# Optimization experiments

Measured on AMD Instinct MI355X. Metric: run time of the kernel, lower is better.

The kernel has to match this reference:

```python
import jax, jax.numpy as jnp
import numpy as np
from jax import lax

B, DZ, H, U, T, V = 256, 512, 512, 16, 16, 512  # batch, latent, lstm hidden, segments, steps/segment, vocab


def setup_inputs() -> dict:
    key = jax.random.key(0)
    ks = jax.random.split(key, 32)
    w = lambda k, shape: jax.random.normal(k, shape, jnp.float32) * 0.05
    d = {
        'z': jax.random.normal(ks[0], (B, DZ), jnp.float32),
        'x': jax.random.randint(ks[1], (B, U * T), 0, V),
        # conductor init-state projection: DZ -> 4H
        'Wc': w(ks[2], (4 * H, DZ)), 'bc': jnp.zeros((4 * H,), jnp.float32),
        # conductor 2-layer LSTM (input H, hidden H)
        'cWih0': w(ks[3], (4 * H, H)), 'cWhh0': w(ks[4], (4 * H, H)),
        'cbih0': jnp.zeros((4 * H,), jnp.float32), 'cbhh0': jnp.zeros((4 * H,), jnp.float32),
        'cWih1': w(ks[5], (4 * H, H)), 'cWhh1': w(ks[6], (4 * H, H)),
        'cbih1': jnp.zeros((4 * H,), jnp.float32), 'cbhh1': jnp.zeros((4 * H,), jnp.float32),
        # decoder init-state projection: H -> 4H
        'Wd': w(ks[7], (4 * H, H)), 'bd': jnp.zeros((4 * H,), jnp.float32),
        # decoder 2-layer LSTM (layer0 input 2H, layer1 input H, hidden H)
        'dWih0': w(ks[8], (4 * H, 2 * H)), 'dWhh0': w(ks[9], (4 * H, H)),
        'dbih0': jnp.zeros((4 * H,), jnp.float32), 'dbhh0': jnp.zeros((4 * H,), jnp.float32),
        'dWih1': w(ks[10], (4 * H, H)), 'dWhh1': w(ks[11], (4 * H, H)),
        'dbih1': jnp.zeros((4 * H,), jnp.float32), 'dbhh1': jnp.zeros((4 * H,), jnp.float32),
        # token embedding and output distribution head
        'emb': w(ks[12], (V, H)),
        'Wo': w(ks[13], (V, H)), 'bo': jnp.zeros((V,), jnp.float32),
    }
    return d


def _cell(x, h, c, Wih, Whh, bih, bhh):
    # PyTorch LSTM gate order: i, f, g, o
    g = x @ Wih.T + bih + h @ Whh.T + bhh
    i, f, gg, o = jnp.split(g, 4, axis=-1)
    c = jax.nn.sigmoid(f) * c + jax.nn.sigmoid(i) * jnp.tanh(gg)
    h = jax.nn.sigmoid(o) * jnp.tanh(c)
    return h, c


def _lstm_layer(xp, h0, c0, Whh, bhh):
    # xp: [N, T, 4H] = precomputed x @ Wih.T + bih
    def step(carry, xg):
        h, c = carry
        g = xg + h @ Whh.T + bhh
        i, f, gg, o = jnp.split(g, 4, axis=-1)
        c = jax.nn.sigmoid(f) * c + jax.nn.sigmoid(i) * jnp.tanh(gg)
        h = jax.nn.sigmoid(o) * jnp.tanh(c)
        return (h, c), h
    _, ys = lax.scan(step, (h0, c0), jnp.swapaxes(xp, 0, 1))
    return jnp.swapaxes(ys, 0, 1)  # [N, T, H]


def reference(z, x, Wc, bc, cWih0, cWhh0, cbih0, cbhh0, cWih1, cWhh1, cbih1, cbhh1,
              Wd, bd, dWih0, dWhh0, dbih0, dbhh0, dWih1, dWhh1, dbih1, dbhh1,
              emb, Wo, bo):
    Bz = z.shape[0]
    # --- conductor ---
    ci = jnp.tanh(z @ Wc.T + bc)  # [B, 4H]
    h1, h2, c1, c2 = ci[:, :H], ci[:, H:2 * H], ci[:, 2 * H:3 * H], ci[:, 3 * H:]
    o0 = jnp.zeros((Bz, H), ci.dtype)

    def cstep(carry, _):
        o, h1, c1, h2, c2 = carry
        h1, c1 = _cell(o, h1, c1, cWih0, cWhh0, cbih0, cbhh0)
        h2, c2 = _cell(h1, h2, c2, cWih1, cWhh1, cbih1, cbhh1)
        return (h2, h1, c1, h2, c2), h2

    _, couts = lax.scan(cstep, (o0, h1, c1, h2, c2), None, length=U)
    cond_out = jnp.swapaxes(couts, 0, 1)  # [B, U, H]

    # --- decoder init states ---
    states = jnp.tanh(cond_out @ Wd.T + bd).reshape(Bz * U, 4 * H)
    dh1, dh2, dc1, dc2 = (states[:, :H], states[:, H:2 * H],
                          states[:, 2 * H:3 * H], states[:, 3 * H:])
    h_init = dh1 + dh2  # [BU, H]

    # --- teacher-forced decoder ---
    xt = x.reshape(Bz * U, T)
    e = emb[xt]  # [BU, T, H]
    e = jnp.concatenate([jnp.zeros((Bz * U, 1, H), e.dtype), e[:, :-1]], axis=1)
    inp = jnp.concatenate(
        [e, jnp.broadcast_to(h_init[:, None], (Bz * U, T, H))], axis=-1)  # [BU, T, 2H]

    y0 = _lstm_layer(inp @ dWih0.T + dbih0, dh1, dc1, dWhh0, dbhh0)
    y1 = _lstm_layer(y0 @ dWih1.T + dbih1, dh2, dc2, dWhh1, dbhh1)
    dist = jax.nn.softmax(y1 @ Wo.T + bo, axis=-1)  # [BU, T, V]
    return dist.reshape(Bz, U * T, V)
```

## Files before the change

### kernel.cpp

```cpp
#include <hip/hip_runtime.h>
#include <math.h>

#define AS1 __attribute__((address_space(1)))
#define AS3 __attribute__((address_space(3)))

typedef __attribute__((ext_vector_type(8))) short short8v;
typedef __attribute__((ext_vector_type(16))) float f32x16;

constexpr size_t PA4c = (size_t)4096 * 512;
constexpr size_t PABc = (size_t)256 * 512;

__device__ __forceinline__ float sigmoidf_(float x) { return 1.f / (1.f + expf(-x)); }
__device__ __forceinline__ unsigned int f2bfu(float f) {
    unsigned int u = __float_as_uint(f);
    return (u + 0x7FFF + ((u >> 16) & 1)) >> 16;
}
__device__ __forceinline__ float bf2f(unsigned int s) { return __uint_as_float(s << 16); }
__device__ __forceinline__ unsigned int pack2(float v) {
    unsigned int b0 = f2bfu(v);
    unsigned int b1 = f2bfu(v - bf2f(b0));
    return b0 | (b1 << 16);
}
__device__ __forceinline__ float unpack2(unsigned int p) { return bf2f(p & 0xffffu) + bf2f(p >> 16); }

__device__ __forceinline__ void xswz(int d, int ngx, int ngy, int& bx, int& by) {
    int nwg = ngx * ngy;
    int q = nwg >> 3, r = nwg & 7, xcd = d & 7, pos = d >> 3;
    int logical = (xcd < r ? xcd * (q + 1) : r * (q + 1) + (xcd - r) * q) + pos;
    bx = logical % ngx; by = logical / ngx;
}

__device__ __forceinline__ size_t offf(int m, int k) {
    return ((size_t)((m >> 5) * 64 + (k >> 3))) * 256 + (size_t)((m & 31) * 8 + (k & 7));
}

template<int N>
__device__ __forceinline__ void wait_vm() {
    asm volatile("s_waitcnt vmcnt(%0) lgkmcnt(0)" :: "n"(N) : "memory");
}

template<int FM, int FN>
__device__ __forceinline__ void gemm_core(
    const short* __restrict__ A1, const short* __restrict__ B1,
    const short* __restrict__ A2, const short* __restrict__ B2,
    int M, int N, int nsteps, int pairSwitch,
    int bx, int by, short* lds, f32x16 (&acc)[FM][FN])
{
    constexpr int ABLK = 4 * FM, BBLK = 2 * FN;
    constexpr int ACH = 2 * ABLK * 2, BCH = 2 * BBLK * 2;
    constexpr int CHT = ACH + BCH;
    constexpr int CPW = CHT / 8;
    constexpr int NBUF = 3;
    constexpr int BUFSH = CHT * 512;
    const int tid = threadIdx.x, lane = tid & 63, wid = tid >> 6;
    const int wm = wid >> 1, wn = wid & 1;
    const int l31 = lane & 31, loct = lane >> 5;
    const int mblk0 = by * ABLK, nblk0 = bx * BBLK;
    const size_t planeA = (size_t)M * 512, planeB = (size_t)N * 512;

    const short* cur[CPW];
    const short* nxt[CPW];
    int ldo[CPW];
    #pragma unroll
    for (int i = 0; i < CPW; ++i) {
        int c = wid * CPW + i;
        ldo[i] = c * 512;
        size_t off;
        const short *b1, *b2;
        if (c < ACH) {
            int plane = c / (ABLK * 2), rem = c % (ABLK * 2), blk = rem >> 1, piece = rem & 1;
            off = (size_t)plane * planeA + (size_t)(mblk0 + blk) * 16384 + piece * 512 + lane * 8;
            b1 = A1; b2 = A2;
        } else {
            int cb = c - ACH;
            int plane = cb / (BBLK * 2), rem = cb % (BBLK * 2), blk = rem >> 1, piece = rem & 1;
            off = (size_t)plane * planeB + (size_t)(nblk0 + blk) * 16384 + piece * 512 + lane * 8;
            b1 = B1; b2 = B2;
        }
        cur[i] = b1 + off;
        nxt[i] = b2 ? (b2 + off) : (b1 + off);
    }

    #pragma unroll
    for (int fm = 0; fm < FM; ++fm)
        #pragma unroll
        for (int fn = 0; fn < FN; ++fn)
            acc[fm][fn] = (f32x16){};

    auto STAGE = [&](int bufIdx) {
        short* db = lds + bufIdx * BUFSH;
        #pragma unroll
        for (int i = 0; i < CPW; ++i) {
            __builtin_amdgcn_global_load_lds((const AS1 unsigned int*)cur[i],
                                             (AS3 unsigned int*)(db + ldo[i]), 16, 0, 0);
            cur[i] += 1024;
        }
    };

    STAGE(0); STAGE(1);
    wait_vm<CPW>();
    __builtin_amdgcn_s_barrier();

    for (int t = 0; t < nsteps; ++t) {
        int s = t + NBUF - 1;
        if (s < nsteps) {
            if (s == pairSwitch) {
                #pragma unroll
                for (int i = 0; i < CPW; ++i) cur[i] = nxt[i];
            }
            STAGE(s % NBUF);
        }
        const short* L = lds + (t % NBUF) * BUFSH;
        #pragma unroll
        for (int ksub = 0; ksub < 2; ++ksub) {
            short8v a[FM][2], b[FN][2];
            #pragma unroll
            for (int p = 0; p < 2; ++p) {
                #pragma unroll
                for (int f = 0; f < FM; ++f)
                    a[f][p] = *(const short8v*)(L + (p * (ABLK * 2) + (wm * FM + f) * 2 + ksub) * 512
                                                  + loct * 256 + l31 * 8);
                #pragma unroll
                for (int f = 0; f < FN; ++f)
                    b[f][p] = *(const short8v*)(L + (ACH + p * (BBLK * 2) + (wn * FN + f) * 2 + ksub) * 512
                                                  + loct * 256 + l31 * 8);
            }
            #pragma unroll
            for (int pp = 0; pp < 3; ++pp) {
                const int pa = (pp == 2) ? 1 : 0, pb = (pp == 1) ? 1 : 0;
                #pragma unroll
                for (int fm = 0; fm < FM; ++fm)
                    #pragma unroll
                    for (int fn = 0; fn < FN; ++fn)
                        acc[fm][fn] = __builtin_amdgcn_mfma_f32_32x32x16_bf16(
                            a[fm][pa], b[fn][pb], acc[fm][fn], 0, 0, 0);
            }
        }
        if (t + 2 < nsteps) wait_vm<CPW>();
        else                wait_vm<0>();
        __builtin_amdgcn_s_barrier();
    }
}

template<int FM, int FN>
__device__ __forceinline__ void gemm_core16(
    const short* __restrict__ A1, const short* __restrict__ B1,
    const short* __restrict__ A2, const short* __restrict__ B2,
    int M, int N, int nsteps, int pairSwitch,
    int bx, int by, short* lds, f32x16 (&acc)[FM][FN])
{
    constexpr int ABLK = 4 * FM, BBLK = 2 * FN;
    constexpr int ACH = 2 * ABLK;
    constexpr int CHT = ACH + 2 * BBLK;
    constexpr int CPW = CHT / 8;
    constexpr int NBUF = 3;
    constexpr int BUFSH = CHT * 512;
    const int tid = threadIdx.x, lane = tid & 63, wid = tid >> 6;
    const int wm = wid >> 1, wn = wid & 1;
    const int l31 = lane & 31, loct = lane >> 5;
    const int mblk0 = by * ABLK, nblk0 = bx * BBLK;
    const size_t planeA = (size_t)M * 512, planeB = (size_t)N * 512;

    const short* cur[CPW];
    const short* nxt[CPW];
    int ldo[CPW];
    #pragma unroll
    for (int i = 0; i < CPW; ++i) {
        int c = wid * CPW + i;
        ldo[i] = c * 512;
        size_t off;
        const short *b1, *b2;
        if (c < ACH) {
            int plane = c / ABLK, blk = c % ABLK;
            off = (size_t)plane * planeA + (size_t)(mblk0 + blk) * 16384 + lane * 8;
            b1 = A1; b2 = A2;
        } else {
            int cb = c - ACH;
            int plane = cb / BBLK, blk = cb % BBLK;
            off = (size_t)plane * planeB + (size_t)(nblk0 + blk) * 16384 + lane * 8;
            b1 = B1; b2 = B2;
        }
        cur[i] = b1 + off;
        nxt[i] = b2 ? (b2 + off) : (b1 + off);
    }

    #pragma unroll
    for (int fm = 0; fm < FM; ++fm)
        #pragma unroll
        for (int fn = 0; fn < FN; ++fn)
            acc[fm][fn] = (f32x16){};

    auto STAGE = [&](int bufIdx) {
        short* db = lds + bufIdx * BUFSH;
        #pragma unroll
        for (int i = 0; i < CPW; ++i) {
            __builtin_amdgcn_global_load_lds((const AS1 unsigned int*)cur[i],
                                             (AS3 unsigned int*)(db + ldo[i]), 16, 0, 0);
            cur[i] += 512;
        }
    };

    STAGE(0); STAGE(1);
    wait_vm<CPW>();
    __builtin_amdgcn_s_barrier();

    for (int t = 0; t < nsteps; ++t) {
        int s = t + NBUF - 1;
        if (s < nsteps) {
            if (s == pairSwitch) {
                #pragma unroll
                for (int i = 0; i < CPW; ++i) cur[i] = nxt[i];
            }
            STAGE(s % NBUF);
        }
        const short* L = lds + (t % NBUF) * BUFSH;
        short8v a[FM][2], b[FN][2];
        #pragma unroll
        for (int p = 0; p < 2; ++p) {
            #pragma unroll
            for (int f = 0; f < FM; ++f)
                a[f][p] = *(const short8v*)(L + (p * ABLK + wm * FM + f) * 512 + loct * 256 + l31 * 8);
            #pragma unroll
            for (int f = 0; f < FN; ++f)
                b[f][p] = *(const short8v*)(L + (ACH + p * BBLK + wn * FN + f) * 512 + loct * 256 + l31 * 8);
        }
        #pragma unroll
        for (int pp = 0; pp < 3; ++pp) {
            const int pa = (pp == 2) ? 1 : 0, pb = (pp == 1) ? 1 : 0;
            #pragma unroll
            for (int fm = 0; fm < FM; ++fm)
                #pragma unroll
                for (int fn = 0; fn < FN; ++fn)
                    acc[fm][fn] = __builtin_amdgcn_mfma_f32_32x32x16_bf16(
                        a[fm][pa], b[fn][pb], acc[fm][fn], 0, 0, 0);
        }
        if (t + 2 < nsteps) wait_vm<CPW>();
        else                wait_vm<0>();
        __builtin_amdgcn_s_barrier();
    }
}

template<int FM, int FN>
__device__ __forceinline__ void epi_f32(f32x16 (&acc)[FM][FN], int bx, int by, int N,
                                        float* __restrict__ Cout, const float* __restrict__ bias, int act)
{
    constexpr int ROWS = 128 * FM, COLS = 64 * FN;
    const int tid = threadIdx.x, lane = tid & 63, wid = tid >> 6;
    const int wm = wid >> 1, wn = wid & 1, l31 = lane & 31, loct = lane >> 5;
    #pragma unroll
    for (int fm = 0; fm < FM; ++fm)
        #pragma unroll
        for (int fn = 0; fn < FN; ++fn) {
            int col = bx * COLS + wn * FN * 32 + fn * 32 + l31;
            int rb  = by * ROWS + wm * FM * 32 + fm * 32 + 4 * loct;
            #pragma unroll
            for (int reg = 0; reg < 16; ++reg) {
                int row = rb + (reg & 3) + 8 * (reg >> 2);
                float xv = acc[fm][fn][reg] + (bias ? bias[row] : 0.f);
                if (act) xv = tanhf(xv);
                Cout[(size_t)row * N + col] = xv;
            }
        }
}

template<int FM, int FN>
__device__ __forceinline__ void epi_pack(f32x16 (&acc)[FM][FN], int bx, int by, int N,
                                         unsigned int* __restrict__ packOut)
{
    constexpr int ROWS = 128 * FM, COLS = 64 * FN;
    const int tid = threadIdx.x, lane = tid & 63, wid = tid >> 6;
    const int wm = wid >> 1, wn = wid & 1, l31 = lane & 31, loct = lane >> 5;
    uint4* P4 = (uint4*)packOut;
    #pragma unroll
    for (int fm = 0; fm < FM; ++fm)
        #pragma unroll
        for (int fn = 0; fn < FN; ++fn) {
            int col = bx * COLS + wn * FN * 32 + fn * 32 + l31;
            int ub = by * (ROWS / 4) + wm * FM * 8 + fm * 8 + loct;
            #pragma unroll
            for (int ug = 0; ug < 4; ++ug) {
                int u = ub + 2 * ug;
                uint4 v;
                v.x = pack2(acc[fm][fn][4 * ug + 0]);
                v.y = pack2(acc[fm][fn][4 * ug + 1]);
                v.z = pack2(acc[fm][fn][4 * ug + 2]);
                v.w = pack2(acc[fm][fn][4 * ug + 3]);
                P4[(size_t)u * N + col] = v;
            }
        }
}

template<int FM, int FN>
__device__ __forceinline__ void epi_gate2(
    f32x16 (&acc)[FM][FN], int bx, int by, int N, short* hl,
    const float* __restrict__ bab,
    const unsigned int* __restrict__ hgP,
    const unsigned int* __restrict__ embT,
    const int* __restrict__ xidx,
    float* __restrict__ cT,
    short* __restrict__ hout, size_t hps,
    short* __restrict__ condp, int ustep)
{
    constexpr int ABLK = 4 * FM, BBLK = 2 * FN;
    constexpr int ROWS = 32 * ABLK, COLS = 32 * BBLK;
    constexpr int CHN = ABLK * BBLK * 256;
    const int tid = threadIdx.x, lane = tid & 63, wid = tid >> 6;
    const int wm = wid >> 1, wn = wid & 1, l31 = lane & 31, loct = lane >> 5;
    #pragma unroll
    for (int fm = 0; fm < FM; ++fm) {
        #pragma unroll
        for (int fn = 0; fn < FN; ++fn) {
            const int col = bx * COLS + wn * FN * 32 + fn * 32 + l31;
            const int ub = by * (ROWS / 4) + wm * FM * 8 + fm * 8 + loct;
            int tok = -1;
            if (xidx) tok = xidx[(size_t)col * 16];
            uint4 hv[4]; uint4 ev[4]; float cv[4]; float4 bv[4];
            #pragma unroll
            for (int ug = 0; ug < 4; ++ug) {
                int u = ub + 2 * ug;
                bv[ug] = *(const float4*)&bab[4 * u];
                cv[ug] = cT[(size_t)u * N + col];
                if (hgP) hv[ug] = ((const uint4*)hgP)[(size_t)u * N + col];
            }
            if (embT && tok >= 0) {
                #pragma unroll
                for (int ug = 0; ug < 4; ++ug) {
                    int u = ub + 2 * ug;
                    ev[ug] = ((const uint4*)embT)[(size_t)u * 512 + tok];
                }
            }
            #pragma unroll
            for (int ug = 0; ug < 4; ++ug) {
                int u = ub + 2 * ug;
                float gi = acc[fm][fn][4 * ug + 0] + bv[ug].x;
                float gf = acc[fm][fn][4 * ug + 1] + bv[ug].y;
                float gg = acc[fm][fn][4 * ug + 2] + bv[ug].z;
                float go = acc[fm][fn][4 * ug + 3] + bv[ug].w;
                if (hgP) {
                    gi += unpack2(hv[ug].x); gf += unpack2(hv[ug].y);
                    gg += unpack2(hv[ug].z); go += unpack2(hv[ug].w);
                }
                if (embT && tok >= 0) {
                    gi += unpack2(ev[ug].x); gf += unpack2(ev[ug].y);
                    gg += unpack2(ev[ug].z); go += unpack2(ev[ug].w);
                }
                float c = sigmoidf_(gf) * cv[ug] + sigmoidf_(gi) * tanhf(gg);
                cT[(size_t)u * N + col] = c;
                float h = sigmoidf_(go) * tanhf(c);
                unsigned int p01 = pack2(h);
                int u_loc = wm * FM * 8 + fm * 8 + loct + 2 * ug;
                int m_loc = wn * FN * 32 + fn * 32 + l31;
                int offl = ((m_loc >> 5) * ABLK + (u_loc >> 3)) * 256 + (m_loc & 31) * 8 + (u_loc & 7);
                hl[offl] = (short)(p01 & 0xffffu);
                hl[CHN + offl] = (short)(p01 >> 16);
                if (condp) {
                    int np = col * 16 + ustep;
                    size_t oc = offf(np, u);
                    condp[oc] = (short)(p01 & 0xffffu);
                    condp[PA4c + oc] = (short)(p01 >> 16);
                }
            }
        }
    }
    __syncthreads();
    constexpr int LB = (ABLK == 8) ? 3 : 2;
    for (int p = 0; p < 2; ++p) {
        for (int jj = tid; jj < CHN / 8; jj += 512) {
            int lc = jj >> 5, m31 = jj & 31;
            int m5 = lc >> LB, u3 = lc & (ABLK - 1);
            size_t gc = (size_t)((bx * BBLK + m5) * 64 + by * ABLK + u3);
            *(short8v*)(hout + p * hps + gc * 256 + m31 * 8) = *(const short8v*)(hl + p * CHN + jj * 8);
        }
    }
}

template<int FM, int FN>
__global__ __launch_bounds__(512, 1) void gemm_packk(
    const short* A1, const short* B1, const short* A2, const short* B2,
    int M, int N, int nsteps, int psw, unsigned int* packOut)
{
    __shared__ __align__(16) short lds[3 * (2 * (4 * FM) * 2 + 2 * (2 * FN) * 2) * 512];
    int d = blockIdx.y * gridDim.x + blockIdx.x;
    int bx, by; xswz(d, gridDim.x, gridDim.y, bx, by);
    f32x16 acc[FM][FN];
    gemm_core<FM, FN>(A1, B1, A2, B2, M, N, nsteps, psw, bx, by, lds, acc);
    epi_pack<FM, FN>(acc, bx, by, N, packOut);
}

template<int FM, int FN>
__global__ __launch_bounds__(512, 1) void gemm_split(
    const short* A1, const short* B1, int M, int N, int nsteps,
    const float* bias, short* hA, short* hB, size_t ps, float* cA, float* cB)
{
    __shared__ __align__(16) short lds[3 * (2 * (4 * FM) * 2 + 2 * (2 * FN) * 2) * 512];
    int d = blockIdx.y * gridDim.x + blockIdx.x;
    int bx, by; xswz(d, gridDim.x, gridDim.y, bx, by);
    f32x16 acc[FM][FN];
    gemm_core<FM, FN>(A1, B1, nullptr, nullptr, M, N, nsteps, 100, bx, by, lds, acc);
    constexpr int ROWS = 128 * FM, COLS = 64 * FN;
    const int tid = threadIdx.x, lane = tid & 63, wid = tid >> 6;
    const int wm = wid >> 1, wn = wid & 1, l31 = lane & 31, loct = lane >> 5;
    #pragma unroll
    for (int fm = 0; fm < FM; ++fm)
        #pragma unroll
        for (int fn = 0; fn < FN; ++fn) {
            int col = bx * COLS + wn * FN * 32 + fn * 32 + l31;
            int rb  = by * ROWS + wm * FM * 32 + fm * 32 + 4 * loct;
            #pragma unroll
            for (int reg = 0; reg < 16; ++reg) {
                int row = rb + (reg & 3) + 8 * (reg >> 2);
                float xv = tanhf(acc[fm][fn][reg] + bias[row]);
                if (row < 1024) {
                    short* hp = (row < 512) ? hA : hB;
                    size_t o = offf(col, row & 511);
                    unsigned int p01 = pack2(xv);
                    hp[o] = (short)(p01 & 0xffffu);
                    hp[ps + o] = (short)(p01 >> 16);
                } else {
                    float* cp = (row < 1536) ? cA : cB;
                    cp[(size_t)(row & 511) * N + col] = xv;
                }
            }
        }
}

__global__ void plane_add(const short* __restrict__ a, const short* __restrict__ b,
                          short* __restrict__ o)
{
    int n8 = (int)(PA4c / 8);
    for (int i = blockIdx.x * 256 + threadIdx.x; i < n8; i += gridDim.x * 256) {
        short8v ah = ((const short8v*)a)[i];
        short8v al = ((const short8v*)(a + PA4c))[i];
        short8v bh = ((const short8v*)b)[i];
        short8v bl = ((const short8v*)(b + PA4c))[i];
        short8v oh, ol;
        #pragma unroll
        for (int j = 0; j < 8; ++j) {
            float v = bf2f((unsigned short)ah[j]) + bf2f((unsigned short)al[j])
                    + bf2f((unsigned short)bh[j]) + bf2f((unsigned short)bl[j]);
            unsigned int p = pack2(v);
            oh[j] = (short)(p & 0xffffu);
            ol[j] = (short)(p >> 16);
        }
        ((short8v*)o)[i] = oh;
        ((short8v*)(o + PA4c))[i] = ol;
    }
}

__global__ __launch_bounds__(512, 1) void cond_cell(
    const short* A1, const short* B1, const short* A2, const short* B2,
    int nsteps, int psw,
    const float* bab, float* cT,
    short* hout, short* condp, int ustep)
{
    __shared__ __align__(16) short lds[3 * 24 * 512];
    int d = blockIdx.y * gridDim.x + blockIdx.x;
    int bx, by; xswz(d, gridDim.x, gridDim.y, bx, by);
    f32x16 acc[1][1];
    gemm_core<1, 1>(A1, B1, A2, B2, 2048, 256, nsteps, psw, bx, by, lds, acc);
    epi_gate2<1, 1>(acc, bx, by, 256, lds, bab, nullptr, nullptr, nullptr,
                    cT, hout, PABc, condp, ustep);
}

struct DecArgs {
    const short *dWhh0P, *dW2P, *dWih1P, *dWhh1P, *WoP, *hiP;
    const float *babd0, *babd1, *bo;
    const unsigned int *embT;
    const int* x;
    float *c0T, *c1dT;
    short *h0a, *h0b, *h1da, *h1db;
    float *LgA, *LgB;
    float* out;
    int t;
};

__global__ __launch_bounds__(512, 1) void dec_step(DecArgs A)
{
    __shared__ __align__(16) short lds[3 * 24 * 512];
    const int role = blockIdx.x >> 8;
    const int dd = blockIdx.x & 255;
    const int t = A.t;
    short* h0[2]  = { A.h0a, A.h0b };
    short* h1d[2] = { A.h1da, A.h1db };
    float* Lg[2]  = { A.LgA, A.LgB };

    if (role == 0) {
        if (t <= 15) {
            int pin = t & 1;
            int bx, by; xswz(dd, 32, 8, bx, by);
            f32x16 acc[2][2];
            gemm_core16<2, 2>(A.dWhh0P, h0[pin], A.dW2P, A.hiP,
                              2048, 4096, 64, 32, bx, by, lds, acc);
            epi_gate2<2, 2>(acc, bx, by, 4096, lds, A.babd0, nullptr,
                            t > 0 ? A.embT : nullptr, t > 0 ? A.x + (t - 1) : nullptr,
                            A.c0T, h0[pin ^ 1], PA4c, nullptr, 0);
            __syncthreads();
        }
        if (t >= 2 && t <= 17) {
            int k = t - 2;
            int bx, by; xswz(dd, 64, 4, bx, by);
            f32x16 acc1[1][1];
            gemm_core<1, 1>(A.WoP, h1d[(k + 1) & 1], nullptr, nullptr, 512, 4096, 16, 100, bx, by, lds, acc1);
            epi_f32<1, 1>(acc1, bx, by, 4096, Lg[k & 1], nullptr, 0);
        }
    } else {
        if (t >= 1 && t <= 16) {
            int s = t - 1;
            int pin2 = s & 1;
            int bx, by; xswz(dd, 32, 8, bx, by);
            f32x16 acc[2][2];
            gemm_core16<2, 2>(A.dWih1P, h0[(s + 1) & 1], A.dWhh1P, h1d[pin2],
                              2048, 4096, 64, 32, bx, by, lds, acc);
            epi_gate2<2, 2>(acc, bx, by, 4096, lds, A.babd1, nullptr, nullptr, nullptr,
                            A.c1dT, h1d[pin2 ^ 1], PA4c, nullptr, 0);
            __syncthreads();
        }
        if (t >= 3) {
            int k = t - 3;
            const float* Lsrc = Lg[k & 1];
            float* tile = (float*)lds;
            float* red  = (float*)lds + 16 * 513;
            float* red2 = red + 512;
            const int tid = threadIdx.x;
            const int mj = tid & 15, vs = tid >> 4;
            const int m = dd * 16 + mj;
            float lv[16];
            #pragma unroll
            for (int i = 0; i < 16; ++i) {
                int v = vs * 16 + i;
                lv[i] = Lsrc[(size_t)v * 4096 + m] + A.bo[v];
            }
            float mx = lv[0];
            #pragma unroll
            for (int i = 1; i < 16; ++i) mx = fmaxf(mx, lv[i]);
            red[vs * 16 + mj] = mx;
            __syncthreads();
            for (int o = 16; o >= 1; o >>= 1) {
                if (vs < o) red[vs * 16 + mj] = fmaxf(red[vs * 16 + mj], red[(vs + o) * 16 + mj]);
                __syncthreads();
            }
            mx = red[mj];
            float sum = 0.f;
            #pragma unroll
            for (int i = 0; i < 16; ++i) {
                float e = expf(lv[i] - mx);
                sum += e;
                tile[mj * 513 + vs * 16 + i] = e;
            }
            red2[vs * 16 + mj] = sum;
            __syncthreads();
            for (int o = 16; o >= 1; o >>= 1) {
                if (vs < o) red2[vs * 16 + mj] += red2[(vs + o) * 16 + mj];
                __syncthreads();
            }
            const int r = tid >> 5, c = tid & 31;
            float invr = 1.f / red2[r];
            for (int kk = 0; kk < 16; ++kk) {
                int v = kk * 32 + c;
                A.out[((size_t)(dd * 16 + r) * 16 + k) * 512 + v] = tile[r * 513 + v] * invr;
            }
        }
    }
}

struct PrepEnt { const float* src; const float* src2; void* dst; int ldw, col0, perm, total, op; };
struct PrepArgs { PrepEnt e[18]; int n; };

__global__ void prep_all(PrepArgs pa)
{
    for (int ei = 0; ei < pa.n; ++ei) {
        PrepEnt E = pa.e[ei];
        for (int o = blockIdx.x * 256 + threadIdx.x; o < E.total; o += gridDim.x * 256) {
            if (E.op == 0) {
                int c = o >> 8, w = o & 255, r = w >> 3, jj = w & 7;
                int n = (c >> 6) * 32 + r, k = (c & 63) * 8 + jj;
                int nsrc = E.perm ? ((n >> 2) + 512 * (n & 3)) : n;
                float v = E.src[(size_t)nsrc * E.ldw + E.col0 + k];
                unsigned int b0 = f2bfu(v);
                short* pl = (short*)E.dst;
                pl[o] = (short)b0;
                pl[E.total + o] = (short)f2bfu(v - bf2f(b0));
            } else {
                int src = (o >> 2) + 512 * (o & 3);
                ((float*)E.dst)[o] = E.src[src] + E.src2[src];
            }
        }
    }
}

extern "C" void kernel_launch(void* const* d_in, const int* in_sizes, int n_in,
                              void* d_out, int out_size, void* d_ws, size_t ws_size,
                              hipStream_t stream)
{
    const float* z     = (const float*)d_in[0];
    const int*   x     = (const int*)  d_in[1];
    const float* Wc    = (const float*)d_in[2];
    const float* bc    = (const float*)d_in[3];
    const float* cWih0 = (const float*)d_in[4];
    const float* cWhh0 = (const float*)d_in[5];
    const float* cbih0 = (const float*)d_in[6];
    const float* cbhh0 = (const float*)d_in[7];
    const float* cWih1 = (const float*)d_in[8];
    const float* cWhh1 = (const float*)d_in[9];
    const float* cbih1 = (const float*)d_in[10];
    const float* cbhh1 = (const float*)d_in[11];
    const float* Wd    = (const float*)d_in[12];
    const float* bd    = (const float*)d_in[13];
    const float* dWih0 = (const float*)d_in[14];
    const float* dWhh0 = (const float*)d_in[15];
    const float* dbih0 = (const float*)d_in[16];
    const float* dbhh0 = (const float*)d_in[17];
    const float* dWih1 = (const float*)d_in[18];
    const float* dWhh1 = (const float*)d_in[19];
    const float* dbih1 = (const float*)d_in[20];
    const float* dbhh1 = (const float*)d_in[21];
    const float* emb   = (const float*)d_in[22];
    const float* Wo    = (const float*)d_in[23];
    const float* bo    = (const float*)d_in[24];
    float* out = (float*)d_out;
    (void)in_sizes; (void)n_in; (void)out_size; (void)ws_size;

    char* wsb = (char*)d_ws;
    size_t off = 0;
    auto alloc = [&](size_t bytes) -> void* {
        off = (off + 255) & ~(size_t)255;
        void* p = wsb + off;
        off += bytes;
        return p;
    };
    const size_t PW  = (size_t)2048 * 512;
    const size_t PWo = (size_t)512 * 512;

    short* WcP    = (short*)alloc(2 * PW * 2);
    short* WdP    = (short*)alloc(2 * PW * 2);
    short* dW1P   = (short*)alloc(2 * PW * 2);
    short* dW2P   = (short*)alloc(2 * PW * 2);
    short* cWih0P = (short*)alloc(2 * PW * 2);
    short* cWhh0P = (short*)alloc(2 * PW * 2);
    short* cWih1P = (short*)alloc(2 * PW * 2);
    short* cWhh1P = (short*)alloc(2 * PW * 2);
    short* dWhh0P = (short*)alloc(2 * PW * 2);
    short* dWih1P = (short*)alloc(2 * PW * 2);
    short* dWhh1P = (short*)alloc(2 * PW * 2);
    short* WoP    = (short*)alloc(2 * PWo * 2);
    short* zpl    = (short*)alloc(2 * PABc * 2);
    short* embpl  = (short*)alloc(2 * PWo * 2);
    float* babc0  = (float*)alloc(2048 * 4);
    float* babc1  = (float*)alloc(2048 * 4);
    float* babd0  = (float*)alloc(2048 * 4);
    float* babd1  = (float*)alloc(2048 * 4);
    float* GbufT  = (float*)alloc((size_t)2048 * 4096 * 4);
    unsigned int* embW0P = (unsigned int*)alloc((size_t)512 * 512 * 4 * 4);
    short* hipl   = (short*)alloc(2 * PA4c * 2);
    short* h1pl[2]; short* h2pl[2];
    h1pl[0] = (short*)alloc(2 * PABc * 2);  h1pl[1] = (short*)alloc(2 * PABc * 2);
    h2pl[0] = (short*)alloc(2 * PABc * 2);  h2pl[1] = (short*)alloc(2 * PABc * 2);
    float* c1T = (float*)alloc((size_t)512 * 256 * 4);
    float* c2T = (float*)alloc((size_t)512 * 256 * 4);
    short* condpl = (short*)alloc(2 * PA4c * 2);
    short* h0pl[2];  short* h1dpl[2];
    h0pl[0]  = (short*)alloc(2 * PA4c * 2); h0pl[1]  = (short*)alloc(2 * PA4c * 2);
    h1dpl[0] = (short*)alloc(2 * PA4c * 2); h1dpl[1] = (short*)alloc(2 * PA4c * 2);
    float* c0T  = (float*)alloc((size_t)512 * 4096 * 4);
    float* c1dT = (float*)alloc((size_t)512 * 4096 * 4);

    float* Lg[2] = { GbufT, GbufT + (size_t)512 * 4096 };

    PrepArgs pa; pa.n = 18;
    auto W8 = [](const float* s, void* d, int ldw, int col0, int perm, int total) {
        PrepEnt e; e.src = s; e.src2 = nullptr; e.dst = d; e.ldw = ldw; e.col0 = col0;
        e.perm = perm; e.total = total; e.op = 0; return e;
    };
    auto B8 = [](const float* a, const float* b, void* d) {
        PrepEnt e; e.src = a; e.src2 = b; e.dst = d; e.ldw = 0; e.col0 = 0;
        e.perm = 0; e.total = 2048; e.op = 1; return e;
    };
    pa.e[0]  = W8(Wc,    WcP,    512,  0,   0, 2048 * 512);
    pa.e[1]  = W8(Wd,    WdP,    512,  0,   0, 2048 * 512);
    pa.e[2]  = W8(dWih0, dW1P,   1024, 0,   1, 2048 * 512);
    pa.e[3]  = W8(dWih0, dW2P,   1024, 512, 1, 2048 * 512);
    pa.e[4]  = W8(cWih0, cWih0P, 512,  0,   1, 2048 * 512);
    pa.e[5]  = W8(cWhh0, cWhh0P, 512,  0,   1, 2048 * 512);
    pa.e[6]  = W8(cWih1, cWih1P, 512,  0,   1, 2048 * 512);
    pa.e[7]  = W8(cWhh1, cWhh1P, 512,  0,   1, 2048 * 512);
    pa.e[8]  = W8(dWhh0, dWhh0P, 512,  0,   1, 2048 * 512);
    pa.e[9]  = W8(dWih1, dWih1P, 512,  0,   1, 2048 * 512);
    pa.e[10] = W8(dWhh1, dWhh1P, 512,  0,   1, 2048 * 512);
    pa.e[11] = W8(Wo,    WoP,    512,  0,   0, 512 * 512);
    pa.e[12] = W8(z,     zpl,    512,  0,   0, 256 * 512);
    pa.e[13] = W8(emb,   embpl,  512,  0,   0, 512 * 512);
    pa.e[14] = B8(cbih0, cbhh0, babc0);
    pa.e[15] = B8(cbih1, cbhh1, babc1);
    pa.e[16] = B8(dbih0, dbhh0, babd0);
    pa.e[17] = B8(dbih1, dbhh1, babd1);
    prep_all<<<dim3(1024), dim3(256), 0, stream>>>(pa);

    gemm_split<2, 2><<<dim3(2, 8), dim3(512), 0, stream>>>(
        WcP, zpl, 2048, 256, 16, bc, h1pl[0], h2pl[0], PABc, c1T, c2T);

    gemm_packk<2, 2><<<dim3(4, 8), dim3(512), 0, stream>>>(
        dW1P, embpl, nullptr, nullptr, 2048, 512, 16, 100, embW0P);

    for (int u = 0; u < 16; ++u) {
        int pin = u & 1;
        if (u == 0)
            cond_cell<<<dim3(4, 16), dim3(512), 0, stream>>>(
                cWhh0P, h1pl[0], nullptr, nullptr, 16, 100,
                babc0, c1T, h1pl[1], nullptr, 0);
        else
            cond_cell<<<dim3(4, 16), dim3(512), 0, stream>>>(
                cWih0P, h2pl[pin], cWhh0P, h1pl[pin], 32, 16,
                babc0, c1T, h1pl[pin ^ 1], nullptr, 0);
        cond_cell<<<dim3(4, 16), dim3(512), 0, stream>>>(
            cWih1P, h1pl[pin ^ 1], cWhh1P, h2pl[pin], 32, 16,
            babc1, c2T, h2pl[pin ^ 1], condpl, u);
    }

    gemm_split<2, 2><<<dim3(32, 8), dim3(512), 0, stream>>>(
        WdP, condpl, 2048, 4096, 16, bd, h0pl[0], h1dpl[0], PA4c, c0T, c1dT);

    plane_add<<<dim3(1024), dim3(256), 0, stream>>>(h0pl[0], h1dpl[0], hipl);

    for (int t = 0; t <= 18; ++t) {
        DecArgs A;
        A.dWhh0P = dWhh0P; A.dW2P = dW2P; A.dWih1P = dWih1P; A.dWhh1P = dWhh1P;
        A.WoP = WoP; A.hiP = hipl;
        A.babd0 = babd0; A.babd1 = babd1; A.bo = bo;
        A.embT = embW0P; A.x = x;
        A.c0T = c0T; A.c1dT = c1dT;
        A.h0a = h0pl[0]; A.h0b = h0pl[1]; A.h1da = h1dpl[0]; A.h1db = h1dpl[1];
        A.LgA = Lg[0]; A.LgB = Lg[1];
        A.out = out; A.t = t;
        dec_step<<<dim3(512), dim3(512), 0, stream>>>(A);
    }
}
```

Baseline: 2.796 ms.

## Precompute time-invariant h_init gate contribution once and deepen decoder GEMM pipeline

Result: faster. 2.523 ms (-9.8%).

```diff
diff --git a/kernel.cpp b/kernel.cpp
--- a/kernel.cpp
+++ b/kernel.cpp
@@ -28,6 +28,13 @@
     int q = nwg >> 3, r = nwg & 7, xcd = d & 7, pos = d >> 3;
     int logical = (xcd < r ? xcd * (q + 1) : r * (q + 1) + (xcd - r) * q) + pos;
     bx = logical % ngx; by = logical / ngx;
+}
+
+__device__ __forceinline__ void xswz_col(int d, int ngx, int ngy, int& bx, int& by) {
+    int cpx = ngx >> 3;
+    int xcd = d & 7, j = d >> 3;
+    bx = xcd * cpx + (j % cpx);
+    by = j / cpx;
 }
 
 __device__ __forceinline__ size_t offf(int m, int k) {
@@ -143,7 +150,7 @@
 }
 
 template<int FM, int FN>
-__device__ __forceinline__ void gemm_core16(
+__device__ __forceinline__ void gemm_core16d(
     const short* __restrict__ A1, const short* __restrict__ B1,
     const short* __restrict__ A2, const short* __restrict__ B2,
     int M, int N, int nsteps, int pairSwitch,
@@ -153,7 +160,7 @@
     constexpr int ACH = 2 * ABLK;
     constexpr int CHT = ACH + 2 * BBLK;
     constexpr int CPW = CHT / 8;
-    constexpr int NBUF = 3;
+    constexpr int NBUF = 6;
     constexpr int BUFSH = CHT * 512;
     const int tid = threadIdx.x, lane = tid & 63, wid = tid >> 6;
     const int wm = wid >> 1, wn = wid & 1;
@@ -200,8 +207,9 @@
         }
     };
 
-    STAGE(0); STAGE(1);
-    wait_vm<CPW>();
+    #pragma unroll
+    for (int i = 0; i < NBUF - 1; ++i) STAGE(i);
+    wait_vm<CPW * (NBUF - 2)>();
     __builtin_amdgcn_s_barrier();
 
     for (int t = 0; t < nsteps; ++t) {
@@ -224,6 +232,7 @@
             for (int f = 0; f < FN; ++f)
                 b[f][p] = *(const short8v*)(L + (ACH + p * BBLK + wn * FN + f) * 512 + loct * 256 + l31 * 8);
         }
+        __builtin_amdgcn_s_setprio(1);
         #pragma unroll
         for (int pp = 0; pp < 3; ++pp) {
             const int pa = (pp == 2) ? 1 : 0, pb = (pp == 1) ? 1 : 0;
@@ -234,8 +243,13 @@
                     acc[fm][fn] = __builtin_amdgcn_mfma_f32_32x32x16_bf16(
                         a[fm][pa], b[fn][pb], acc[fm][fn], 0, 0, 0);
         }
-        if (t + 2 < nsteps) wait_vm<CPW>();
-        else                wait_vm<0>();
+        __builtin_amdgcn_s_setprio(0);
+        int rem = nsteps - 2 - t;
+        if (rem >= 4)      wait_vm<CPW * 4>();
+        else if (rem == 3) wait_vm<CPW * 3>();
+        else if (rem == 2) wait_vm<CPW * 2>();
+        else if (rem == 1) wait_vm<CPW * 1>();
+        else               wait_vm<0>();
         __builtin_amdgcn_s_barrier();
     }
 }
@@ -377,11 +391,13 @@
 template<int FM, int FN>
 __global__ __launch_bounds__(512, 1) void gemm_packk(
     const short* A1, const short* B1, const short* A2, const short* B2,
-    int M, int N, int nsteps, int psw, unsigned int* packOut)
+    int M, int N, int nsteps, int psw, int colmap, unsigned int* packOut)
 {
     __shared__ __align__(16) short lds[3 * (2 * (4 * FM) * 2 + 2 * (2 * FN) * 2) * 512];
     int d = blockIdx.y * gridDim.x + blockIdx.x;
-    int bx, by; xswz(d, gridDim.x, gridDim.y, bx, by);
+    int bx, by;
+    if (colmap) xswz_col(d, gridDim.x, gridDim.y, bx, by);
+    else        xswz(d, gridDim.x, gridDim.y, bx, by);
     f32x16 acc[FM][FN];
     gemm_core<FM, FN>(A1, B1, A2, B2, M, N, nsteps, psw, bx, by, lds, acc);
     epi_pack<FM, FN>(acc, bx, by, N, packOut);
@@ -389,12 +405,14 @@
 
 template<int FM, int FN>
 __global__ __launch_bounds__(512, 1) void gemm_split(
-    const short* A1, const short* B1, int M, int N, int nsteps,
+    const short* A1, const short* B1, int M, int N, int nsteps, int colmap,
     const float* bias, short* hA, short* hB, size_t ps, float* cA, float* cB)
 {
     __shared__ __align__(16) short lds[3 * (2 * (4 * FM) * 2 + 2 * (2 * FN) * 2) * 512];
     int d = blockIdx.y * gridDim.x + blockIdx.x;
-    int bx, by; xswz(d, gridDim.x, gridDim.y, bx, by);
+    int bx, by;
+    if (colmap) xswz_col(d, gridDim.x, gridDim.y, bx, by);
+    else        xswz(d, gridDim.x, gridDim.y, bx, by);
     f32x16 acc[FM][FN];
     gemm_core<FM, FN>(A1, B1, nullptr, nullptr, M, N, nsteps, 100, bx, by, lds, acc);
     constexpr int ROWS = 128 * FM, COLS = 64 * FN;
@@ -424,29 +442,6 @@
         }
 }
 
-__global__ void plane_add(const short* __restrict__ a, const short* __restrict__ b,
-                          short* __restrict__ o)
-{
-    int n8 = (int)(PA4c / 8);
-    for (int i = blockIdx.x * 256 + threadIdx.x; i < n8; i += gridDim.x * 256) {
-        short8v ah = ((const short8v*)a)[i];
-        short8v al = ((const short8v*)(a + PA4c))[i];
-        short8v bh = ((const short8v*)b)[i];
-        short8v bl = ((const short8v*)(b + PA4c))[i];
-        short8v oh, ol;
-        #pragma unroll
-        for (int j = 0; j < 8; ++j) {
-            float v = bf2f((unsigned short)ah[j]) + bf2f((unsigned short)al[j])
-                    + bf2f((unsigned short)bh[j]) + bf2f((unsigned short)bl[j]);
-            unsigned int p = pack2(v);
-            oh[j] = (short)(p & 0xffffu);
-            ol[j] = (short)(p >> 16);
-        }
-        ((short8v*)o)[i] = oh;
-        ((short8v*)(o + PA4c))[i] = ol;
-    }
-}
-
 __global__ __launch_bounds__(512, 1) void cond_cell(
     const short* A1, const short* B1, const short* A2, const short* B2,
     int nsteps, int psw,
@@ -463,9 +458,9 @@
 }
 
 struct DecArgs {
-    const short *dWhh0P, *dW2P, *dWih1P, *dWhh1P, *WoP, *hiP;
+    const short *dWhh0P, *dWih1P, *dWhh1P, *WoP;
     const float *babd0, *babd1, *bo;
-    const unsigned int *embT;
+    const unsigned int *hgP, *embT;
     const int* x;
     float *c0T, *c1dT;
     short *h0a, *h0b, *h1da, *h1db;
@@ -476,7 +471,7 @@
 
 __global__ __launch_bounds__(512, 1) void dec_step(DecArgs A)
 {
-    __shared__ __align__(16) short lds[3 * 24 * 512];
+    __shared__ __align__(16) short lds[6 * 24 * 512];
     const int role = blockIdx.x >> 8;
     const int dd = blockIdx.x & 255;
     const int t = A.t;
@@ -487,18 +482,17 @@
     if (role == 0) {
         if (t <= 15) {
             int pin = t & 1;
-            int bx, by; xswz(dd, 32, 8, bx, by);
+            int bx, by; xswz_col(dd, 32, 8, bx, by);
             f32x16 acc[2][2];
-            gemm_core16<2, 2>(A.dWhh0P, h0[pin], A.dW2P, A.hiP,
-                              2048, 4096, 64, 32, bx, by, lds, acc);
-            epi_gate2<2, 2>(acc, bx, by, 4096, lds, A.babd0, nullptr,
+            gemm_core16d<2, 2>(A.dWhh0P, h0[pin], nullptr, nullptr, 2048, 4096, 32, 100, bx, by, lds, acc);
+            epi_gate2<2, 2>(acc, bx, by, 4096, lds, A.babd0, A.hgP,
                             t > 0 ? A.embT : nullptr, t > 0 ? A.x + (t - 1) : nullptr,
                             A.c0T, h0[pin ^ 1], PA4c, nullptr, 0);
             __syncthreads();
         }
         if (t >= 2 && t <= 17) {
             int k = t - 2;
-            int bx, by; xswz(dd, 64, 4, bx, by);
+            int bx, by; xswz_col(dd, 64, 4, bx, by);
             f32x16 acc1[1][1];
             gemm_core<1, 1>(A.WoP, h1d[(k + 1) & 1], nullptr, nullptr, 512, 4096, 16, 100, bx, by, lds, acc1);
             epi_f32<1, 1>(acc1, bx, by, 4096, Lg[k & 1], nullptr, 0);
@@ -507,10 +501,10 @@
         if (t >= 1 && t <= 16) {
             int s = t - 1;
             int pin2 = s & 1;
-            int bx, by; xswz(dd, 32, 8, bx, by);
+            int bx, by; xswz_col(dd, 32, 8, bx, by);
             f32x16 acc[2][2];
-            gemm_core16<2, 2>(A.dWih1P, h0[(s + 1) & 1], A.dWhh1P, h1d[pin2],
-                              2048, 4096, 64, 32, bx, by, lds, acc);
+            gemm_core16d<2, 2>(A.dWih1P, h0[(s + 1) & 1], A.dWhh1P, h1d[pin2],
+                               2048, 4096, 64, 32, bx, by, lds, acc);
             epi_gate2<2, 2>(acc, bx, by, 4096, lds, A.babd1, nullptr, nullptr, nullptr,
                             A.c1dT, h1d[pin2 ^ 1], PA4c, nullptr, 0);
             __syncthreads();
@@ -650,8 +644,8 @@
     float* babd0  = (float*)alloc(2048 * 4);
     float* babd1  = (float*)alloc(2048 * 4);
     float* GbufT  = (float*)alloc((size_t)2048 * 4096 * 4);
-    unsigned int* embW0P = (unsigned int*)alloc((size_t)512 * 512 * 4 * 4);
-    short* hipl   = (short*)alloc(2 * PA4c * 2);
+    unsigned int* hinitgP = (unsigned int*)alloc((size_t)512 * 4096 * 4 * 4);
+    unsigned int* embW0P  = (unsigned int*)alloc((size_t)512 * 512 * 4 * 4);
     short* h1pl[2]; short* h2pl[2];
     h1pl[0] = (short*)alloc(2 * PABc * 2);  h1pl[1] = (short*)alloc(2 * PABc * 2);
     h2pl[0] = (short*)alloc(2 * PABc * 2);  h2pl[1] = (short*)alloc(2 * PABc * 2);
@@ -696,10 +690,10 @@
     prep_all<<<dim3(1024), dim3(256), 0, stream>>>(pa);
 
     gemm_split<2, 2><<<dim3(2, 8), dim3(512), 0, stream>>>(
-        WcP, zpl, 2048, 256, 16, bc, h1pl[0], h2pl[0], PABc, c1T, c2T);
+        WcP, zpl, 2048, 256, 16, 0, bc, h1pl[0], h2pl[0], PABc, c1T, c2T);
 
     gemm_packk<2, 2><<<dim3(4, 8), dim3(512), 0, stream>>>(
-        dW1P, embpl, nullptr, nullptr, 2048, 512, 16, 100, embW0P);
+        dW1P, embpl, nullptr, nullptr, 2048, 512, 16, 100, 0, embW0P);
 
     for (int u = 0; u < 16; ++u) {
         int pin = u & 1;
@@ -717,16 +711,16 @@
     }
 
     gemm_split<2, 2><<<dim3(32, 8), dim3(512), 0, stream>>>(
-        WdP, condpl, 2048, 4096, 16, bd, h0pl[0], h1dpl[0], PA4c, c0T, c1dT);
-
-    plane_add<<<dim3(1024), dim3(256), 0, stream>>>(h0pl[0], h1dpl[0], hipl);
+        WdP, condpl, 2048, 4096, 16, 1, bd, h0pl[0], h1dpl[0], PA4c, c0T, c1dT);
+
+    gemm_packk<2, 2><<<dim3(32, 8), dim3(512), 0, stream>>>(
+        dW2P, h0pl[0], dW2P, h1dpl[0], 2048, 4096, 32, 16, 1, hinitgP);
 
     for (int t = 0; t <= 18; ++t) {
         DecArgs A;
-        A.dWhh0P = dWhh0P; A.dW2P = dW2P; A.dWih1P = dWih1P; A.dWhh1P = dWhh1P;
-        A.WoP = WoP; A.hiP = hipl;
+        A.dWhh0P = dWhh0P; A.dWih1P = dWih1P; A.dWhh1P = dWhh1P; A.WoP = WoP;
         A.babd0 = babd0; A.babd1 = babd1; A.bo = bo;
-        A.embT = embW0P; A.x = x;
+        A.hgP = hinitgP; A.embT = embW0P; A.x = x;
         A.c0T = c0T; A.c1dT = c1dT;
         A.h0a = h0pl[0]; A.h0b = h0pl[1]; A.h1da = h1dpl[0]; A.h1db = h1dpl[1];
         A.LgA = Lg[0]; A.LgB = Lg[1];
```
